# Kernel optimization log

Hardware: AMD Instinct MI355X
Metric: run time of the kernel (lower is better)

The kernel has to match this reference:

```python
import jax, jax.numpy as jnp
import numpy as np

B, S, D, F, E = 2, 1024, 1024, 4096, 8

def setup_inputs() -> dict:
    key = jax.random.key(0)
    ks = jax.random.split(key, 4)
    s = 0.02
    return {
        "x": jax.random.normal(ks[0], (B, S, D), dtype=jnp.float32),
        "switch_w": jax.random.normal(ks[1], (D, E), dtype=jnp.float32) * s,
        "switch_b": jnp.zeros((E,), dtype=jnp.float32),
        "w1": jax.random.normal(ks[2], (E, D, F), dtype=jnp.float32) * s,
        "b1": jnp.zeros((E, F), dtype=jnp.float32),
        "w2": jax.random.normal(ks[3], (E, F, D), dtype=jnp.float32) * s,
        "b2": jnp.zeros((E, D), dtype=jnp.float32),
    }

def reference(x, switch_w, switch_b, w1, b1, w2, b2):
    b, s, d = x.shape
    xt = x.reshape(-1, d)                               # [T, D]
    logits = xt @ switch_w + switch_b                   # [T, E]
    route_prob = jax.nn.softmax(logits, axis=-1)        # [T, E]
    route_prob_max = jnp.max(route_prob, axis=-1)       # [T]
    routes = jnp.argmax(route_prob, axis=-1)            # [T] int
    onehot = jax.nn.one_hot(routes, E, dtype=xt.dtype)  # [T, E]
    counts = onehot.sum(axis=0)                         # tokens per expert (float, as in torch new_tensor)

    # top-1 dispatch: run each expert FFN, keep only its tokens via mask (drop_tokens=False -> no capacity drop)
    def body(acc, params):
        W1, B1, W2, B2, mask = params                   # mask: [T]
        y = jax.nn.relu(xt @ W1 + B1) @ W2 + B2         # [T, D]
        return acc + mask[:, None] * y, None

    out, _ = jax.lax.scan(body, jnp.zeros_like(xt), (w1, b1, w2, b2, onehot.T))
    out = out * route_prob_max[:, None]                 # is_scale_prob=True
    final_output = out.reshape(b, s, d)
    return final_output, counts, route_prob.sum(axis=0), 0, route_prob_max
```

## Files before the change

### kernel.cpp

```cpp
#include <hip/hip_runtime.h>
#include <stdint.h>

#define T_TOK 2048
#define D_DIM 1024
#define F_DIM 4096
#define E_NUM 8
#define RPMAX 3072
#define BK 64

typedef __attribute__((ext_vector_type(8))) short bfx8;
typedef __attribute__((ext_vector_type(4))) float fx4;

__device__ __forceinline__ unsigned short f2bf(float f) {
  union { float f; uint32_t u; } v; v.f = f;
  uint32_t u = v.u;
  u += 0x7FFFu + ((u >> 16) & 1u);
  return (unsigned short)(u >> 16);
}

__device__ __forceinline__ void load_lds16(const unsigned short* g, unsigned short* l) {
  __builtin_amdgcn_global_load_lds(
      (const __attribute__((address_space(1))) void*)g,
      (__attribute__((address_space(3))) void*)l, 16, 0, 0);
}

__device__ __forceinline__ uint32_t cvtpk_bf16(float lo, float hi) {
  uint32_t d;
  asm("v_cvt_pk_bf16_f32 %0, %1, %2" : "=v"(d) : "v"(lo), "v"(hi));
  return d;
}

template <int N>
__device__ __forceinline__ void vm_wait_lgkm() {
  if constexpr (N == 0) asm volatile("s_waitcnt vmcnt(0) lgkmcnt(0)" ::: "memory");
  else if constexpr (N == 8) asm volatile("s_waitcnt vmcnt(8) lgkmcnt(0)" ::: "memory");
  else if constexpr (N == 12) asm volatile("s_waitcnt vmcnt(12) lgkmcnt(0)" ::: "memory");
}

__global__ __launch_bounds__(256) void router_kernel(
    const float* __restrict__ x, const float* __restrict__ sw,
    const float* __restrict__ sb, float* __restrict__ pmax_out,
    int* __restrict__ routes, float* __restrict__ probs,
    unsigned short* __restrict__ xbf) {
  const int wave = threadIdx.x >> 6, lane = threadIdx.x & 63;
  const int t = blockIdx.x * 4 + wave;
  const float* xr = x + (size_t)t * D_DIM;
  float acc[8];
#pragma unroll
  for (int e = 0; e < 8; ++e) acc[e] = 0.f;
#pragma unroll
  for (int i = 0; i < 4; ++i) {
    const int d = i * 256 + lane * 4;
    float4 xv = *(const float4*)(xr + d);
    ushort4 h;
    h.x = f2bf(xv.x); h.y = f2bf(xv.y); h.z = f2bf(xv.z); h.w = f2bf(xv.w);
    *(ushort4*)(xbf + (size_t)t * D_DIM + d) = h;
    const float xs[4] = {xv.x, xv.y, xv.z, xv.w};
#pragma unroll
    for (int j = 0; j < 4; ++j) {
      const float4* swp = (const float4*)(sw + (size_t)(d + j) * 8);
      float4 w0 = swp[0], w1 = swp[1];
      acc[0] += xs[j] * w0.x; acc[1] += xs[j] * w0.y;
      acc[2] += xs[j] * w0.z; acc[3] += xs[j] * w0.w;
      acc[4] += xs[j] * w1.x; acc[5] += xs[j] * w1.y;
      acc[6] += xs[j] * w1.z; acc[7] += xs[j] * w1.w;
    }
  }
#pragma unroll
  for (int e = 0; e < 8; ++e) {
    float v = acc[e];
    for (int o = 32; o > 0; o >>= 1) v += __shfl_down(v, o, 64);
    acc[e] = v;
  }
  if (lane == 0) {
#pragma unroll
    for (int e = 0; e < 8; ++e) acc[e] += sb[e];
    int am = 0; float mx = acc[0];
#pragma unroll
    for (int e = 1; e < 8; ++e) if (acc[e] > mx) { mx = acc[e]; am = e; }
    float p[8]; float s = 0.f;
#pragma unroll
    for (int e = 0; e < 8; ++e) { p[e] = expf(acc[e] - mx); s += p[e]; }
    float inv = 1.0f / s;
    pmax_out[t] = inv;
    routes[t] = am;
#pragma unroll
    for (int e = 0; e < 8; ++e) probs[(size_t)t * 8 + e] = p[e] * inv;
  }
}

__global__ __launch_bounds__(256) void plan_kernel(
    const int* __restrict__ routes, const float* __restrict__ probs,
    int* __restrict__ off, int* __restrict__ cursor,
    int* __restrict__ perm_out, int* __restrict__ perm_src,
    float* __restrict__ out_counts, float* __restrict__ out_psums,
    float* __restrict__ out_zero) {
  __shared__ int cnt[8];
  __shared__ float red[256][8];
  const int tid = threadIdx.x;
  if (tid < 8) { cnt[tid] = 0; cursor[tid] = 0; }
  for (int i = tid; i < RPMAX; i += 256) { perm_out[i] = -1; perm_src[i] = 0; }
  __syncthreads();
  float loc[8];
#pragma unroll
  for (int e = 0; e < 8; ++e) loc[e] = 0.f;
  for (int t = tid; t < T_TOK; t += 256) {
    atomicAdd(&cnt[routes[t]], 1);
    const float4* p = (const float4*)(probs + (size_t)t * 8);
    float4 a = p[0], b = p[1];
    loc[0] += a.x; loc[1] += a.y; loc[2] += a.z; loc[3] += a.w;
    loc[4] += b.x; loc[5] += b.y; loc[6] += b.z; loc[7] += b.w;
  }
#pragma unroll
  for (int e = 0; e < 8; ++e) red[tid][e] = loc[e];
  __syncthreads();
  for (int s = 128; s >= 1; s >>= 1) {
    if (tid < s) {
#pragma unroll
      for (int e = 0; e < 8; ++e) red[tid][e] += red[tid + s][e];
    }
    __syncthreads();
  }
  if (tid == 0) {
    int o = 0;
    for (int e = 0; e < 8; ++e) { off[e] = o; o += ((cnt[e] + 127) >> 7) << 7; }
    off[8] = o;
    *out_zero = 0.0f;
  }
  if (tid < 8) {
    out_counts[tid] = (float)cnt[tid];
    out_psums[tid] = red[0][tid];
  }
}

__global__ __launch_bounds__(256) void scatter_kernel(
    const int* __restrict__ routes, const int* __restrict__ off,
    int* __restrict__ cursor, int* __restrict__ perm_out,
    int* __restrict__ perm_src) {
  int t = blockIdx.x * 256 + threadIdx.x;
  if (t >= T_TOK) return;
  int e = routes[t];
  int pos = atomicAdd(&cursor[e], 1);
  perm_out[off[e] + pos] = t;
  perm_src[off[e] + pos] = t;
}

template <int K_, int N_, bool FIRST, bool NCHUNK>
__global__ __launch_bounds__(256, 2) void gemm_fused(
    const unsigned short* __restrict__ A,
    const float* __restrict__ W,
    const float* __restrict__ Bias,
    const int* __restrict__ off,
    const int* __restrict__ perm_src, const int* __restrict__ perm_out,
    const float* __restrict__ pmax,
    unsigned short* __restrict__ Hout, float* __restrict__ Out) {
  constexpr int NT = K_ / BK;
  __shared__ __align__(16) unsigned short As[3][128 * 64];
  __shared__ __align__(16) unsigned short Bs[2][64 * 64];
  const int tid = threadIdx.x;
  const int nbx = gridDim.x, nby = gridDim.y;
  const int lin = blockIdx.y * nbx + blockIdx.x;
  const int chunkg = (nbx * nby) >> 3;
  const int newlin = (lin & 7) * chunkg + (lin >> 3);
  const int bx = NCHUNK ? (newlin / nby) : (newlin % nbx);
  const int by = NCHUNK ? (newlin % nby) : (newlin / nbx);
  const int rowbase = by * 128;
  if (rowbase >= off[8]) return;
  int e = 0;
#pragma unroll
  for (int i = 1; i <= 7; ++i) if (rowbase >= off[i]) e = i;
  const int n0 = bx * 64;
  const int wave = tid >> 6, lane = tid & 63;
  const int wm = wave >> 1, wn = wave & 1;
  const float* Wn0 = W + (size_t)e * K_ * N_ + n0;

  const unsigned short* aSrc[4];
#pragma unroll
  for (int c = 0; c < 4; ++c) {
    int ca = (wave * 4 + c) * 64 + lane;
    int row = ca >> 3, slot = ca & 7;
    int sc = slot ^ (row & 7);
    size_t arow = FIRST ? (size_t)perm_src[rowbase + row] : (size_t)(rowbase + row);
    aSrc[c] = A + arow * K_ + sc * 8;
  }

  const int nq = lane & 15;
  const int qg = lane >> 4;
  fx4 bregE[4], bregO[4];

  auto A_STAGE = [&](int kt, unsigned short* Asb) {
#pragma unroll
    for (int c = 0; c < 4; ++c)
      load_lds16(aSrc[c] + kt, Asb + (wave * 4 + c) * 512);
  };
  auto B_LOAD = [&](int kt, fx4* br) {
#pragma unroll
    for (int j = 0; j < 4; ++j)
      br[j] = *(const fx4*)(Wn0 + (size_t)(kt + wave * 16 + qg * 4 + j) * N_ + nq * 4);
  };
  auto B_STORE = [&](fx4* br, unsigned short* Bsb) {
    const int c16 = wave * 2 + (qg >> 1);
    const int h4 = (qg & 1) * 4;
#pragma unroll
    for (int i = 0; i < 4; ++i) {
      const int nl = nq * 4 + i;
      const int key = ((nl >> 2) + 2 * (nl & 3)) & 7;
      uint32_t d0 = cvtpk_bf16(br[0][i], br[1][i]);
      uint32_t d1 = cvtpk_bf16(br[2][i], br[3][i]);
      *(uint2*)(Bsb + nl * 64 + (c16 ^ key) * 8 + h4) = make_uint2(d0, d1);
    }
  };

  fx4 acc[4][2];
#pragma unroll
  for (int a = 0; a < 4; ++a)
#pragma unroll
    for (int b = 0; b < 2; ++b) acc[a][b] = (fx4){0.f, 0.f, 0.f, 0.f};

  auto COMPUTE = [&](const unsigned short* Asb, const unsigned short* Bsb) {
    __builtin_amdgcn_s_setprio(1);
#pragma unroll
    for (int kk = 0; kk < 2; ++kk) {
      bfx8 af[4], bf[2];
#pragma unroll
      for (int fm = 0; fm < 4; ++fm) {
        int r = wm * 64 + fm * 16 + (lane & 15);
        int c = (kk * 4 + (lane >> 4)) ^ (r & 7);
        af[fm] = *(const bfx8*)(Asb + r * 64 + c * 8);
      }
#pragma unroll
      for (int fn = 0; fn < 2; ++fn) {
        int nn = wn * 32 + fn * 16 + (lane & 15);
        int key = ((nn >> 2) + 2 * (nn & 3)) & 7;
        int c = (kk * 4 + (lane >> 4)) ^ key;
        bf[fn] = *(const bfx8*)(Bsb + nn * 64 + c * 8);
      }
#pragma unroll
      for (int fm = 0; fm < 4; ++fm)
#pragma unroll
        for (int fn = 0; fn < 2; ++fn)
          acc[fm][fn] = __builtin_amdgcn_mfma_f32_16x16x32_bf16(
              af[fm], bf[fn], acc[fm][fn], 0, 0, 0);
    }
    __builtin_amdgcn_s_setprio(0);
  };

  unsigned short *a0 = As[0], *a1 = As[1], *a2 = As[2];

  A_STAGE(0, a0);
  __builtin_amdgcn_sched_barrier(0);
  B_LOAD(0, bregE);
  __builtin_amdgcn_sched_barrier(0);
  A_STAGE(BK, a1);
  __builtin_amdgcn_sched_barrier(0);
  B_LOAD(BK, bregO);
  B_STORE(bregE, Bs[0]);
  vm_wait_lgkm<8>();
  __builtin_amdgcn_s_barrier();

  for (int t = 0; t < NT - 2; t += 2) {
    A_STAGE((t + 2) * BK, a2);
    __builtin_amdgcn_sched_barrier(0);
    B_LOAD((t + 2) * BK, bregE);
    COMPUTE(a0, Bs[0]);
    B_STORE(bregO, Bs[1]);
    vm_wait_lgkm<8>();
    __builtin_amdgcn_s_barrier();
    { unsigned short* tmp = a0; a0 = a1; a1 = a2; a2 = tmp; }
    if (t + 3 < NT) {
      A_STAGE((t + 3) * BK, a2);
      __builtin_amdgcn_sched_barrier(0);
      B_LOAD((t + 3) * BK, bregO);
    }
    COMPUTE(a0, Bs[1]);
    B_STORE(bregE, Bs[0]);
    vm_wait_lgkm<8>();
    __builtin_amdgcn_s_barrier();
    { unsigned short* tmp = a0; a0 = a1; a1 = a2; a2 = tmp; }
  }
  COMPUTE(a0, Bs[0]);
  B_STORE(bregO, Bs[1]);
  vm_wait_lgkm<0>();
  __builtin_amdgcn_s_barrier();
  { unsigned short* tmp = a0; a0 = a1; a1 = a2; a2 = tmp; }
  COMPUTE(a0, Bs[1]);

  const int colbase = n0 + wn * 32;
  if (FIRST) {
#pragma unroll
    for (int fn = 0; fn < 2; ++fn) {
      int colg = colbase + fn * 16 + (lane & 15);
      float bv = Bias[(size_t)e * N_ + colg];
#pragma unroll
      for (int fm = 0; fm < 4; ++fm) {
        int rg = rowbase + wm * 64 + fm * 16 + ((lane >> 4) << 2);
#pragma unroll
        for (int j = 0; j < 4; ++j) {
          float v = fmaxf(acc[fm][fn][j] + bv, 0.f);
          Hout[(size_t)(rg + j) * N_ + colg] = f2bf(v);
        }
      }
    }
  } else {
#pragma unroll
    for (int fm = 0; fm < 4; ++fm) {
      int rg = rowbase + wm * 64 + fm * 16 + ((lane >> 4) << 2);
#pragma unroll
      for (int j = 0; j < 4; ++j) {
        int tok = perm_out[rg + j];
        if (tok < 0) continue;
        float pm = pmax[tok];
#pragma unroll
        for (int fn = 0; fn < 2; ++fn) {
          int colg = colbase + fn * 16 + (lane & 15);
          Out[(size_t)tok * N_ + colg] = (acc[fm][fn][j] + Bias[(size_t)e * N_ + colg]) * pm;
        }
      }
    }
  }
}

extern "C" void kernel_launch(void* const* d_in, const int* in_sizes, int n_in,
                              void* d_out, int out_size, void* d_ws, size_t ws_size,
                              hipStream_t stream) {
  const float* x  = (const float*)d_in[0];
  const float* sw = (const float*)d_in[1];
  const float* sb = (const float*)d_in[2];
  const float* w1 = (const float*)d_in[3];
  const float* b1 = (const float*)d_in[4];
  const float* w2 = (const float*)d_in[5];
  const float* b2 = (const float*)d_in[6];
  float* out = (float*)d_out;

  char* ws = (char*)d_ws;
  int*   off      = (int*)(ws + 0);
  int*   cursor   = (int*)(ws + 512);
  int*   routes   = (int*)(ws + 1024);
  int*   perm_out = (int*)(ws + 16384);
  int*   perm_src = (int*)(ws + 32768);
  float* probs    = (float*)(ws + 49152);
  unsigned short* xbf = (unsigned short*)(ws + (1u << 20));
  unsigned short* H   = (unsigned short*)(ws + (8u << 20));

  float* out_final  = out;
  float* out_counts = out + 2097152;
  float* out_psums  = out + 2097160;
  float* out_zero   = out + 2097168;
  float* out_pmax   = out + 2097169;

  router_kernel<<<T_TOK / 4, 256, 0, stream>>>(x, sw, sb, out_pmax, routes, probs, xbf);
  plan_kernel<<<1, 256, 0, stream>>>(routes, probs, off, cursor, perm_out, perm_src,
                                     out_counts, out_psums, out_zero);
  scatter_kernel<<<(T_TOK + 255) / 256, 256, 0, stream>>>(routes, off, cursor,
                                                          perm_out, perm_src);

  gemm_fused<D_DIM, F_DIM, true, true>
      <<<dim3(F_DIM / 64, RPMAX / 128), 256, 0, stream>>>(
          xbf, w1, b1, off, perm_src, perm_out, nullptr, H, nullptr);
  gemm_fused<F_DIM, D_DIM, false, false>
      <<<dim3(D_DIM / 64, RPMAX / 128), 256, 0, stream>>>(
          H, w2, b2, off, perm_src, perm_out, out_pmax, nullptr, out_final);
}
```

Baseline: 161.3 us.

## Fuse token scatter into plan kernel and deepen B-weight register prefetch

Moves the per-expert token scatter into the single-block plan kernel, using shared-memory cursors initialised from the computed offsets. This removes one kernel launch and its global atomics. The GEMM main loop now keeps three register sets of B tiles, prefetching weights two K-steps ahead instead of one, with a deeper vmcnt wait. The deeper prefetch aims to hide global fp32 weight-load latency at the cost of more VGPRs, which could cut occupancy or cause spills under launch_bounds(256,2).

```diff
diff --git a/kernel.cpp b/kernel.cpp
--- a/kernel.cpp
+++ b/kernel.cpp
@@ -36,6 +36,7 @@
   else if constexpr (N == 8) asm volatile("s_waitcnt vmcnt(8) lgkmcnt(0)" ::: "memory");
   else if constexpr (N == 12) asm volatile("s_waitcnt vmcnt(12) lgkmcnt(0)" ::: "memory");
 }
+#define SB() __builtin_amdgcn_sched_barrier(0)
 
 __global__ __launch_bounds__(256) void router_kernel(
     const float* __restrict__ x, const float* __restrict__ sw,
@@ -91,14 +92,15 @@
 
 __global__ __launch_bounds__(256) void plan_kernel(
     const int* __restrict__ routes, const float* __restrict__ probs,
-    int* __restrict__ off, int* __restrict__ cursor,
-    int* __restrict__ perm_out, int* __restrict__ perm_src,
+    int* __restrict__ off, int* __restrict__ perm_out, int* __restrict__ perm_src,
     float* __restrict__ out_counts, float* __restrict__ out_psums,
     float* __restrict__ out_zero) {
   __shared__ int cnt[8];
+  __shared__ int cur[8];
+  __shared__ int offs[9];
   __shared__ float red[256][8];
   const int tid = threadIdx.x;
-  if (tid < 8) { cnt[tid] = 0; cursor[tid] = 0; }
+  if (tid < 8) cnt[tid] = 0;
   for (int i = tid; i < RPMAX; i += 256) { perm_out[i] = -1; perm_src[i] = 0; }
   __syncthreads();
   float loc[8];
@@ -123,26 +125,24 @@
   }
   if (tid == 0) {
     int o = 0;
-    for (int e = 0; e < 8; ++e) { off[e] = o; o += ((cnt[e] + 127) >> 7) << 7; }
-    off[8] = o;
+    for (int e = 0; e < 8; ++e) { offs[e] = o; o += ((cnt[e] + 127) >> 7) << 7; }
+    offs[8] = o;
     *out_zero = 0.0f;
   }
+  __syncthreads();
+  if (tid < 9) off[tid] = offs[tid];
   if (tid < 8) {
+    cur[tid] = offs[tid];
     out_counts[tid] = (float)cnt[tid];
     out_psums[tid] = red[0][tid];
   }
-}
-
-__global__ __launch_bounds__(256) void scatter_kernel(
-    const int* __restrict__ routes, const int* __restrict__ off,
-    int* __restrict__ cursor, int* __restrict__ perm_out,
-    int* __restrict__ perm_src) {
-  int t = blockIdx.x * 256 + threadIdx.x;
-  if (t >= T_TOK) return;
-  int e = routes[t];
-  int pos = atomicAdd(&cursor[e], 1);
-  perm_out[off[e] + pos] = t;
-  perm_src[off[e] + pos] = t;
+  __syncthreads();
+  for (int t = tid; t < T_TOK; t += 256) {
+    int e = routes[t];
+    int pos = atomicAdd(&cur[e], 1);
+    perm_out[pos] = t;
+    perm_src[pos] = t;
+  }
 }
 
 template <int K_, int N_, bool FIRST, bool NCHUNK>
@@ -186,7 +186,7 @@
 
   const int nq = lane & 15;
   const int qg = lane >> 4;
-  fx4 bregE[4], bregO[4];
+  fx4 brA[4], brB[4], brT[4];
 
   auto A_STAGE = [&](int kt, unsigned short* Asb) {
 #pragma unroll
@@ -247,42 +247,40 @@
 
   unsigned short *a0 = As[0], *a1 = As[1], *a2 = As[2];
 
-  A_STAGE(0, a0);
-  __builtin_amdgcn_sched_barrier(0);
-  B_LOAD(0, bregE);
-  __builtin_amdgcn_sched_barrier(0);
-  A_STAGE(BK, a1);
-  __builtin_amdgcn_sched_barrier(0);
-  B_LOAD(BK, bregO);
-  B_STORE(bregE, Bs[0]);
+  A_STAGE(0, a0); SB();
+  B_LOAD(0, brT); SB();
+  A_STAGE(BK, a1); SB();
+  B_LOAD(BK, brA); SB();
+  B_LOAD(2 * BK, brB);
+  B_STORE(brT, Bs[0]);
+  vm_wait_lgkm<12>();
+  __builtin_amdgcn_s_barrier();
+
+#pragma unroll 2
+  for (int t = 0; t < NT - 3; ++t) {
+    A_STAGE((t + 2) * BK, a2); SB();
+    B_LOAD((t + 3) * BK, brT);
+    COMPUTE(a0, Bs[t & 1]);
+    B_STORE(brA, Bs[(t + 1) & 1]);
+    vm_wait_lgkm<12>();
+    __builtin_amdgcn_s_barrier();
+    { unsigned short* tmp = a0; a0 = a1; a1 = a2; a2 = tmp; }
+#pragma unroll
+    for (int j = 0; j < 4; ++j) { brA[j] = brB[j]; brB[j] = brT[j]; }
+  }
+  A_STAGE((NT - 1) * BK, a2);
+  COMPUTE(a0, Bs[1]);
+  B_STORE(brA, Bs[0]);
   vm_wait_lgkm<8>();
   __builtin_amdgcn_s_barrier();
-
-  for (int t = 0; t < NT - 2; t += 2) {
-    A_STAGE((t + 2) * BK, a2);
-    __builtin_amdgcn_sched_barrier(0);
-    B_LOAD((t + 2) * BK, bregE);
-    COMPUTE(a0, Bs[0]);
-    B_STORE(bregO, Bs[1]);
-    vm_wait_lgkm<8>();
-    __builtin_amdgcn_s_barrier();
-    { unsigned short* tmp = a0; a0 = a1; a1 = a2; a2 = tmp; }
-    if (t + 3 < NT) {
-      A_STAGE((t + 3) * BK, a2);
-      __builtin_amdgcn_sched_barrier(0);
-      B_LOAD((t + 3) * BK, bregO);
-    }
-    COMPUTE(a0, Bs[1]);
-    B_STORE(bregE, Bs[0]);
-    vm_wait_lgkm<8>();
-    __builtin_amdgcn_s_barrier();
-    { unsigned short* tmp = a0; a0 = a1; a1 = a2; a2 = tmp; }
-  }
+  { unsigned short* tmp = a0; a0 = a1; a1 = a2; a2 = tmp; }
+#pragma unroll
+  for (int j = 0; j < 4; ++j) brA[j] = brB[j];
   COMPUTE(a0, Bs[0]);
-  B_STORE(bregO, Bs[1]);
+  B_STORE(brA, Bs[1]);
   vm_wait_lgkm<0>();
   __builtin_amdgcn_s_barrier();
-  { unsigned short* tmp = a0; a0 = a1; a1 = a2; a2 = tmp; }
+  { unsigned short* tmp = a0; a0 = a1; a1 = tmp; }
   COMPUTE(a0, Bs[1]);
 
   const int colbase = n0 + wn * 32;
@@ -334,7 +332,6 @@
 
   char* ws = (char*)d_ws;
   int*   off      = (int*)(ws + 0);
-  int*   cursor   = (int*)(ws + 512);
   int*   routes   = (int*)(ws + 1024);
   int*   perm_out = (int*)(ws + 16384);
   int*   perm_src = (int*)(ws + 32768);
@@ -349,10 +346,8 @@
   float* out_pmax   = out + 2097169;
 
   router_kernel<<<T_TOK / 4, 256, 0, stream>>>(x, sw, sb, out_pmax, routes, probs, xbf);
-  plan_kernel<<<1, 256, 0, stream>>>(routes, probs, off, cursor, perm_out, perm_src,
+  plan_kernel<<<1, 256, 0, stream>>>(routes, probs, off, perm_out, perm_src,
                                      out_counts, out_psums, out_zero);
-  scatter_kernel<<<(T_TOK + 255) / 256, 256, 0, stream>>>(routes, off, cursor,
-                                                          perm_out, perm_src);
 
   gemm_fused<D_DIM, F_DIM, true, true>
       <<<dim3(F_DIM / 64, RPMAX / 128), 256, 0, stream>>>(
```

Measured after the change: 166.8 us. +3.4%, slower.
